# Optimization experiments

Measured on AMD Instinct MI355X. Metric: run time of the kernel, lower is better.

Reference implementation:

```python
import jax, jax.numpy as jnp
import numpy as np

WINDOW = (7, 7)
SHIFT = (3, 3)
NUM_HEADS = 4
DIM = 128


def _rel_pos_index():
    wh, ww = WINDOW
    coords = np.stack(np.meshgrid(np.arange(wh), np.arange(ww), indexing='ij'))  # [2,wh,ww]
    cf = coords.reshape(2, -1)                    # [2, N]
    rc = (cf[:, :, None] - cf[:, None, :]).transpose(1, 2, 0)  # [N,N,2]
    rc[:, :, 0] += wh - 1
    rc[:, :, 1] += ww - 1
    rc[:, :, 0] *= 2 * ww - 1
    return jnp.asarray(rc.sum(-1).reshape(-1))    # [N*N] int


def _attn_mask_np(pH, pW, sh):
    # Static-shape shift mask (host-side numpy; constant under jit).
    wh, ww = WINDOW
    m = np.zeros((pH, pW))
    h_slices = ((0, pH - wh), (pH - wh, pH - sh[0]), (pH - sh[0], pH))
    w_slices = ((0, pW - ww), (pW - ww, pW - sh[1]), (pW - sh[1], pW))
    cnt = 0
    for hs in h_slices:
        for ws in w_slices:
            m[hs[0]:hs[1], ws[0]:ws[1]] = cnt
            cnt += 1
    m = m.reshape(pH // wh, wh, pW // ww, ww).transpose(0, 2, 1, 3).reshape(-1, wh * ww)
    diff = m[:, None, :] - m[:, :, None]          # [num_windows, N, N]
    return jnp.asarray(np.where(diff != 0, -100.0, 0.0), dtype=np.float32)


def setup_inputs() -> dict:
    key = jax.random.key(0)
    ks = jax.random.split(key, 9)
    B, H, W, C = 32, 56, 56, DIM
    return {
        'input_q': jax.random.normal(ks[0], (B, H, W, C), jnp.float32),
        'input_k': jax.random.normal(ks[1], (B, H, W, C), jnp.float32),
        'input_v': jax.random.normal(ks[2], (B, H, W, C), jnp.float32),
        'q_weight': jax.random.normal(ks[3], (C, C), jnp.float32) * 0.05,
        'q_bias': jnp.zeros((C,), jnp.float32),
        'k_weight': jax.random.normal(ks[4], (C, C), jnp.float32) * 0.05,
        'k_bias': jnp.zeros((C,), jnp.float32),
        'v_weight': jax.random.normal(ks[5], (C, C), jnp.float32) * 0.05,
        'v_bias': jnp.zeros((C,), jnp.float32),
        'proj_weight': jax.random.normal(ks[6], (C, C), jnp.float32) * 0.05,
        'proj_bias': jnp.zeros((C,), jnp.float32),
        'rpb_table': jax.random.normal(ks[7], ((2 * WINDOW[0] - 1) * (2 * WINDOW[1] - 1), NUM_HEADS), jnp.float32) * 0.02,
    }


def reference(input_q, input_k, input_v, q_weight, q_bias, k_weight, k_bias,
              v_weight, v_bias, proj_weight, proj_bias, rpb_table):
    B, H, W, C = input_q.shape
    wh, ww = WINDOW
    pad_b = (wh - H % wh) % wh
    pad_r = (ww - W % ww) % ww
    pad = lambda t: jnp.pad(t, ((0, 0), (0, pad_b), (0, pad_r), (0, 0)))
    qx, kx, vx = pad(input_q), pad(input_k), pad(input_v)
    pad_H, pad_W = H + pad_b, W + pad_r
    sh = [0 if wh >= pad_H else SHIFT[0], 0 if ww >= pad_W else SHIFT[1]]
    if sum(sh) > 0:
        roll = lambda t: jnp.roll(t, (-sh[0], -sh[1]), axis=(1, 2))
        qx, kx, vx = roll(qx), roll(kx), roll(vx)
    nWh, nWw = pad_H // wh, pad_W // ww
    num_windows = nWh * nWw
    N = wh * ww

    def part(t):  # [B,pH,pW,C] -> [B*num_windows, N, C]
        t = t.reshape(B, nWh, wh, nWw, ww, C).transpose(0, 1, 3, 2, 4, 5)
        return t.reshape(B * num_windows, N, C)

    qx, kx, vx = part(qx), part(kx), part(vx)
    hd = C // NUM_HEADS

    def heads(x, w, b):  # linear + split heads -> [BW, nH, N, hd]
        return (x @ w.T + b).reshape(-1, N, NUM_HEADS, hd).transpose(0, 2, 1, 3)

    q = heads(qx, q_weight, q_bias) * (hd ** -0.5)
    k = heads(kx, k_weight, k_bias)
    v = heads(vx, v_weight, v_bias)

    attn = jnp.einsum('whqd,whkd->whqk', q, k)    # [BW, nH, N, N]
    rpb = rpb_table[_rel_pos_index()].reshape(N, N, NUM_HEADS).transpose(2, 0, 1)[None]
    attn = attn + rpb
    if sum(sh) > 0:
        mask = _attn_mask_np(pad_H, pad_W, sh)    # [num_windows, N, N]
        attn = attn.reshape(B, num_windows, NUM_HEADS, N, N) + mask[None, :, None]
        attn = attn.reshape(B * num_windows, NUM_HEADS, N, N)
    attn = jax.nn.softmax(attn, axis=-1)

    x = jnp.einsum('whqk,whkd->whqd', attn, v).transpose(0, 2, 1, 3).reshape(B * num_windows, N, C)
    x = x @ proj_weight.T + proj_bias
    x = x.reshape(B, nWh, nWw, wh, ww, C).transpose(0, 1, 3, 2, 4, 5).reshape(B, pad_H, pad_W, C)
    if sum(sh) > 0:
        x = jnp.roll(x, (sh[0], sh[1]), axis=(1, 2))
    return x[:, :H, :W, :]
```

## Files before the change

kernel.cpp:

```cpp
#include <hip/hip_runtime.h>

typedef __attribute__((ext_vector_type(8))) short s16x8;
typedef __attribute__((ext_vector_type(4))) float f32x4;
typedef __attribute__((ext_vector_type(4))) unsigned int u32x4;

#define MFMA16(a, b, c) __builtin_amdgcn_mfma_f32_16x16x32_bf16((a), (b), (c), 0, 0, 0)

static __device__ __forceinline__ unsigned short f2bf(float f) {
  unsigned int u = __float_as_uint(f);
  u += 0x7fffu + ((u >> 16) & 1u);
  return (unsigned short)(u >> 16);
}
static __device__ __forceinline__ int div7(int x) { return (x * 9363) >> 16; }
static __device__ __forceinline__ int swz256(int row, int byteoff) {
  return row * 256 + (byteoff ^ ((row & 7) << 4));
}
static __device__ __forceinline__ int swz128(int row, int byteoff) {
  return row * 128 + (byteoff ^ ((row & 7) << 4));
}

__global__ void swin_prep(const float* __restrict__ wq, const float* __restrict__ wk,
                          const float* __restrict__ wv, const float* __restrict__ wp,
                          const float* __restrict__ rpb_table,
                          unsigned short* __restrict__ wsW, float* __restrict__ rpbx) {
  int idx = blockIdx.x * 256 + threadIdx.x;
  if (idx < 65536) {
    int t = idx >> 14, loc = idx & 16383;
    const float* s = (t == 0) ? wq : (t == 1) ? wk : (t == 2) ? wv : wp;
    wsW[idx] = f2bf(s[loc]);
  } else {
    int k = idx - 65536;
    if (k < 4 * 49 * 49) {
      int h = k / 2401, rem = k - h * 2401;
      int i = rem / 49, j = rem - i * 49;
      int yi = i / 7, xi = i % 7, yj = j / 7, xj = j % 7;
      int ridx = (yi - yj + 6) * 13 + (xi - xj + 6);
      rpbx[k] = rpb_table[ridx * 4 + h];
    }
  }
}

__global__ __launch_bounds__(512, 4) void swin_main(
    const float* __restrict__ xq, const float* __restrict__ xk, const float* __restrict__ xv,
    const float* __restrict__ bq, const float* __restrict__ bk, const float* __restrict__ bv,
    const float* __restrict__ bp, const unsigned short* __restrict__ wsW,
    const float* __restrict__ rpbx, float* __restrict__ out) {
  __shared__ __align__(16) char sm[65536];

  const int tid = threadIdx.x;
  const int lane = tid & 63;
  const int wv_ = tid >> 6;
  const int l15 = lane & 15;
  const int lg = lane >> 4;
  const int kgrp = lg * 8;
  const int rsub = lg * 4;

  const int bid = blockIdx.x;
  const int b = bid >> 6;
  const int widx = bid & 63;
  const int wi = widx >> 3, wj = widx & 7;
  const long obase = (long)b * 56 * 56 * 128;

  const int xrow = tid >> 3;
  const int xk16 = (tid & 7) << 4;
  long xoff = -1;
  if (xrow < 49) {
    int ty = div7(xrow), tx = xrow - ty * 7;
    int ih = wi * 7 + ty + 3; if (ih >= 56) ih -= 56;
    int iw = wj * 7 + tx + 3; if (iw >= 56) iw -= 56;
    xoff = obase + (long)((ih * 56 + iw) * 128 + xk16);
  }
  float xr[16];
#pragma unroll
  for (int i = 0; i < 16; ++i) xr[i] = 0.f;

  auto issue_x = [&](const float* src) {
    if (xoff >= 0) {
      const float* p = src + xoff;
#pragma unroll
      for (int q = 0; q < 4; ++q) {
        f32x4 v = *(const f32x4*)(p + q * 4);
        xr[q * 4 + 0] = v[0]; xr[q * 4 + 1] = v[1];
        xr[q * 4 + 2] = v[2]; xr[q * 4 + 3] = v[3];
      }
    }
  };
  auto write_x = [&]() {
    unsigned int w[8];
#pragma unroll
    for (int i = 0; i < 8; ++i)
      w[i] = (unsigned int)f2bf(xr[2 * i]) | ((unsigned int)f2bf(xr[2 * i + 1]) << 16);
    u32x4 a = {w[0], w[1], w[2], w[3]};
    u32x4 bb = {w[4], w[5], w[6], w[7]};
    *(u32x4*)(sm + swz256(xrow, xk16 * 2)) = a;
    *(u32x4*)(sm + swz256(xrow, xk16 * 2 + 16)) = bb;
  };

  auto linear = [&](int woff, const float* bias, float scale, int mode, int dstbase) {
    const int n = wv_ * 16 + l15;
    s16x8 bfr[4];
#pragma unroll
    for (int kt = 0; kt < 4; ++kt)
      bfr[kt] = *(const s16x8*)(wsW + woff + n * 128 + kt * 32 + kgrp);
    float bval = bias[n] * scale;
#pragma unroll
    for (int mt = 0; mt < 4; ++mt) {
      f32x4 acc = {0.f, 0.f, 0.f, 0.f};
#pragma unroll
      for (int kt = 0; kt < 4; ++kt) {
        s16x8 afr = *(const s16x8*)(sm + swz256(mt * 16 + l15, (kt * 32 + kgrp) * 2));
        acc = MFMA16(afr, bfr[kt], acc);
      }
#pragma unroll
      for (int r = 0; r < 4; ++r) {
        float val = acc[r] * scale + bval;
        unsigned short h16 = f2bf(val);
        int row = mt * 16 + rsub + r;
        if (mode == 0)
          *(unsigned short*)(sm + dstbase + swz256(row, 2 * n)) = h16;
        else
          *(unsigned short*)(sm + 49152 + swz128(n, 2 * row)) = h16;
      }
    }
  };

  const float QSCALE = 0.17677669529663687f;

  issue_x(xq);
  write_x(); __syncthreads();
  issue_x(xk);
  linear(0, bq, QSCALE, 0, 16384); __syncthreads();
  write_x(); __syncthreads();
  issue_x(xv);
  linear(16384, bk, 1.f, 0, 32768); __syncthreads();
  write_x(); __syncthreads();
  linear(32768, bv, 1.f, 1, 0); __syncthreads();

  {
    const int h = wv_ & 3;
    const int half = wv_ >> 2;
    const int coff = h * 32;

    s16x8 kfr[4];
#pragma unroll
    for (int jt = 0; jt < 4; ++jt)
      kfr[jt] = *(const s16x8*)(sm + 32768 + swz256(jt * 16 + l15, (coff + kgrp) * 2));
    f32x4 S[2][4];
#pragma unroll
    for (int m2 = 0; m2 < 2; ++m2) {
      int mt = half * 2 + m2;
      s16x8 qfr = *(const s16x8*)(sm + 16384 + swz256(mt * 16 + l15, (coff + kgrp) * 2));
#pragma unroll
      for (int jt = 0; jt < 4; ++jt) {
        f32x4 z = {0.f, 0.f, 0.f, 0.f};
        S[m2][jt] = MFMA16(qfr, kfr[jt], z);
      }
    }

    const float* rpbh = rpbx + h * 2401;
    int jj[4], rgj[4]; bool jvld[4];
#pragma unroll
    for (int jt = 0; jt < 4; ++jt) {
      int j = jt * 16 + l15;
      jj[jt] = j; jvld[jt] = (j < 49);
      int jc = jvld[jt] ? j : 0;
      int yj = div7(jc), xj = jc - yj * 7;
      rgj[jt] = ((wi == 7) ? (yj < 4 ? 3 : 6) : 0) + ((wj == 7) ? (xj < 4 ? 1 : 2) : 0);
    }
#pragma unroll
    for (int m2 = 0; m2 < 2; ++m2) {
#pragma unroll
      for (int r = 0; r < 4; ++r) {
        int i = (half * 2 + m2) * 16 + rsub + r;
        if (i < 49) {
          int yi = div7(i), xi = i - yi * 7;
          int rgi = ((wi == 7) ? (yi < 4 ? 3 : 6) : 0) + ((wj == 7) ? (xi < 4 ? 1 : 2) : 0);
#pragma unroll
          for (int jt = 0; jt < 4; ++jt) {
            if (jvld[jt]) {
              float sv = S[m2][jt][r] + rpbh[i * 49 + jj[jt]];
              if (rgi != rgj[jt]) sv -= 100.f;
              S[m2][jt][r] = sv;
            } else {
              S[m2][jt][r] = -1e30f;
            }
          }
        } else {
#pragma unroll
          for (int jt = 0; jt < 4; ++jt)
            if (!jvld[jt]) S[m2][jt][r] = -1e30f;
        }
      }
    }

#pragma unroll
    for (int m2 = 0; m2 < 2; ++m2) {
#pragma unroll
      for (int r = 0; r < 4; ++r) {
        float m = fmaxf(fmaxf(S[m2][0][r], S[m2][1][r]), fmaxf(S[m2][2][r], S[m2][3][r]));
        for (int d = 1; d < 16; d <<= 1) m = fmaxf(m, __shfl_xor(m, d));
        float e0 = __expf(S[m2][0][r] - m);
        float e1 = __expf(S[m2][1][r] - m);
        float e2 = __expf(S[m2][2][r] - m);
        float e3 = __expf(S[m2][3][r] - m);
        float s = e0 + e1 + e2 + e3;
        for (int d = 1; d < 16; d <<= 1) s += __shfl_xor(s, d);
        float inv = 1.0f / s;
        S[m2][0][r] = e0 * inv; S[m2][1][r] = e1 * inv;
        S[m2][2][r] = e2 * inv; S[m2][3][r] = e3 * inv;
      }
    }
    __syncthreads();

    const int pbase = 16384 + h * 8192;
#pragma unroll
    for (int m2 = 0; m2 < 2; ++m2)
#pragma unroll
      for (int r = 0; r < 4; ++r) {
        int i = (half * 2 + m2) * 16 + rsub + r;
#pragma unroll
        for (int jt = 0; jt < 4; ++jt)
          *(unsigned short*)(sm + pbase + swz128(i, 2 * (jt * 16 + l15))) = f2bf(S[m2][jt][r]);
      }
    __syncthreads();

    s16x8 vfr[2][2];
#pragma unroll
    for (int ks = 0; ks < 2; ++ks)
#pragma unroll
      for (int nt = 0; nt < 2; ++nt) {
        int c = coff + nt * 16 + l15;
        vfr[ks][nt] = *(const s16x8*)(sm + 49152 + swz128(c, (ks * 32 + kgrp) * 2));
      }
    f32x4 Oacc[2][2];
#pragma unroll
    for (int m2 = 0; m2 < 2; ++m2)
#pragma unroll
      for (int nt = 0; nt < 2; ++nt) Oacc[m2][nt] = (f32x4){0.f, 0.f, 0.f, 0.f};
#pragma unroll
    for (int m2 = 0; m2 < 2; ++m2) {
#pragma unroll
      for (int ks = 0; ks < 2; ++ks) {
        s16x8 pfr = *(const s16x8*)(sm + pbase + swz128((half * 2 + m2) * 16 + l15, (ks * 32 + kgrp) * 2));
        Oacc[m2][0] = MFMA16(pfr, vfr[ks][0], Oacc[m2][0]);
        Oacc[m2][1] = MFMA16(pfr, vfr[ks][1], Oacc[m2][1]);
      }
    }
#pragma unroll
    for (int m2 = 0; m2 < 2; ++m2)
#pragma unroll
      for (int nt = 0; nt < 2; ++nt)
#pragma unroll
        for (int r = 0; r < 4; ++r) {
          int row = (half * 2 + m2) * 16 + rsub + r;
          int c = coff + nt * 16 + l15;
          *(unsigned short*)(sm + swz256(row, 2 * c)) = f2bf(Oacc[m2][nt][r]);
        }
    __syncthreads();
  }

  {
    const int woff = 49152;
    const int n = wv_ * 16 + l15;
    s16x8 bfr[4];
#pragma unroll
    for (int kt = 0; kt < 4; ++kt)
      bfr[kt] = *(const s16x8*)(wsW + woff + n * 128 + kt * 32 + kgrp);
    float bval = bp[n];
#pragma unroll
    for (int mt = 0; mt < 4; ++mt) {
      f32x4 acc = {0.f, 0.f, 0.f, 0.f};
#pragma unroll
      for (int kt = 0; kt < 4; ++kt) {
        s16x8 afr = *(const s16x8*)(sm + swz256(mt * 16 + l15, (kt * 32 + kgrp) * 2));
        acc = MFMA16(afr, bfr[kt], acc);
      }
#pragma unroll
      for (int r = 0; r < 4; ++r) {
        int tok = mt * 16 + rsub + r;
        if (tok < 49) {
          int ty = div7(tok), tx = tok - ty * 7;
          int oh = wi * 7 + ty + 3; if (oh >= 56) oh -= 56;
          int ow = wj * 7 + tx + 3; if (ow >= 56) ow -= 56;
          out[obase + (oh * 56 + ow) * 128 + n] = acc[r] + bval;
        }
      }
    }
  }
}

extern "C" void kernel_launch(void* const* d_in, const int* in_sizes, int n_in,
                              void* d_out, int out_size, void* d_ws, size_t ws_size,
                              hipStream_t stream) {
  const float* xq = (const float*)d_in[0];
  const float* xk = (const float*)d_in[1];
  const float* xv = (const float*)d_in[2];
  const float* wq = (const float*)d_in[3];
  const float* bq = (const float*)d_in[4];
  const float* wk = (const float*)d_in[5];
  const float* bk = (const float*)d_in[6];
  const float* wv = (const float*)d_in[7];
  const float* bv = (const float*)d_in[8];
  const float* wp = (const float*)d_in[9];
  const float* bp = (const float*)d_in[10];
  const float* rpb = (const float*)d_in[11];

  unsigned short* wsW = (unsigned short*)d_ws;
  float* rpbx = (float*)((char*)d_ws + 131072);

  swin_prep<<<294, 256, 0, stream>>>(wq, wk, wv, wp, rpb, wsW, rpbx);

  float* out = (float*)d_out;
  swin_main<<<2048, 512, 0, stream>>>(xq, xk, xv, bq, bk, bv, bp, wsW, rpbx, out);
}
```

Baseline: 90.65 us.

## Precompute padded bias+mask tables per window case and use exp2 softmax

The prep kernel now builds four padded 64x64 tables per head, one per shift-mask case. Each table folds together the relative position bias, the -100 shift mask, the padding sentinel and a log2(e) scale, so the main kernel only adds a preloaded value instead of computing region indices and branching. The Q scale also absorbs log2(e), so the softmax can use exp2f. The change also packs bf16 conversions in pairs with the hardware intrinsic, removes a barrier by moving the V projection into the attention scope, and hoists the bias loads ahead of the QK MFMAs. The trade-off is a larger bias table to read from global memory and more live registers for the preloaded values.

```diff
diff --git a/kernel.cpp b/kernel.cpp
--- a/kernel.cpp
+++ b/kernel.cpp
@@ -1,15 +1,18 @@
 #include <hip/hip_runtime.h>
+#include <hip/hip_bf16.h>
 
 typedef __attribute__((ext_vector_type(8))) short s16x8;
 typedef __attribute__((ext_vector_type(4))) float f32x4;
+typedef __attribute__((ext_vector_type(2))) unsigned int u32x2;
 typedef __attribute__((ext_vector_type(4))) unsigned int u32x4;
 
 #define MFMA16(a, b, c) __builtin_amdgcn_mfma_f32_16x16x32_bf16((a), (b), (c), 0, 0, 0)
-
-static __device__ __forceinline__ unsigned short f2bf(float f) {
-  unsigned int u = __float_as_uint(f);
-  u += 0x7fffu + ((u >> 16) & 1u);
-  return (unsigned short)(u >> 16);
+#define LOG2E 1.4426950408889634f
+
+static __device__ __forceinline__ unsigned int pk2(float a, float b) {
+  union { __hip_bfloat162 h2; unsigned int u; } cv;
+  cv.h2 = __float22bfloat162_rn(make_float2(a, b));
+  return cv.u;
 }
 static __device__ __forceinline__ int div7(int x) { return (x * 9363) >> 16; }
 static __device__ __forceinline__ int swz256(int row, int byteoff) {
@@ -22,21 +25,34 @@
 __global__ void swin_prep(const float* __restrict__ wq, const float* __restrict__ wk,
                           const float* __restrict__ wv, const float* __restrict__ wp,
                           const float* __restrict__ rpb_table,
-                          unsigned short* __restrict__ wsW, float* __restrict__ rpbx) {
+                          unsigned short* __restrict__ wsW, float* __restrict__ rpbm) {
   int idx = blockIdx.x * 256 + threadIdx.x;
   if (idx < 65536) {
     int t = idx >> 14, loc = idx & 16383;
     const float* s = (t == 0) ? wq : (t == 1) ? wk : (t == 2) ? wv : wp;
-    wsW[idx] = f2bf(s[loc]);
+    union { __hip_bfloat16 h; unsigned short u; } cv;
+    cv.h = __float2bfloat16(s[loc]);
+    wsW[idx] = cv.u;
   } else {
     int k = idx - 65536;
-    if (k < 4 * 49 * 49) {
-      int h = k / 2401, rem = k - h * 2401;
-      int i = rem / 49, j = rem - i * 49;
-      int yi = i / 7, xi = i % 7, yj = j / 7, xj = j % 7;
+    int c = k >> 14;
+    int h = (k >> 12) & 3;
+    int i = (k >> 6) & 63, j = k & 63;
+    float val;
+    if (j >= 49) val = -1e30f;
+    else if (i >= 49) val = 0.f;
+    else {
+      int yi = div7(i), xi = i - yi * 7;
+      int yj = div7(j), xj = j - yj * 7;
       int ridx = (yi - yj + 6) * 13 + (xi - xj + 6);
-      rpbx[k] = rpb_table[ridx * 4 + h];
-    }
+      val = rpb_table[ridx * 4 + h];
+      int cwi = c >> 1, cwj = c & 1;
+      int rgi = (cwi ? (yi < 4 ? 3 : 6) : 0) + (cwj ? (xi < 4 ? 1 : 2) : 0);
+      int rgj = (cwi ? (yj < 4 ? 3 : 6) : 0) + (cwj ? (xj < 4 ? 1 : 2) : 0);
+      if (rgi != rgj) val -= 100.f;
+      val *= LOG2E;
+    }
+    rpbm[k] = val;
   }
 }
 
@@ -44,7 +60,7 @@
     const float* __restrict__ xq, const float* __restrict__ xk, const float* __restrict__ xv,
     const float* __restrict__ bq, const float* __restrict__ bk, const float* __restrict__ bv,
     const float* __restrict__ bp, const unsigned short* __restrict__ wsW,
-    const float* __restrict__ rpbx, float* __restrict__ out) {
+    const float* __restrict__ rpbm, float* __restrict__ out) {
   __shared__ __align__(16) char sm[65536];
 
   const int tid = threadIdx.x;
@@ -60,6 +76,7 @@
   const int widx = bid & 63;
   const int wi = widx >> 3, wj = widx & 7;
   const long obase = (long)b * 56 * 56 * 128;
+  const int mcase = ((wi == 7) ? 2 : 0) + ((wj == 7) ? 1 : 0);
 
   const int xrow = tid >> 3;
   const int xk16 = (tid & 7) << 4;
@@ -88,13 +105,17 @@
   auto write_x = [&]() {
     unsigned int w[8];
 #pragma unroll
-    for (int i = 0; i < 8; ++i)
-      w[i] = (unsigned int)f2bf(xr[2 * i]) | ((unsigned int)f2bf(xr[2 * i + 1]) << 16);
+    for (int i = 0; i < 8; ++i) w[i] = pk2(xr[2 * i], xr[2 * i + 1]);
     u32x4 a = {w[0], w[1], w[2], w[3]};
     u32x4 bb = {w[4], w[5], w[6], w[7]};
     *(u32x4*)(sm + swz256(xrow, xk16 * 2)) = a;
     *(u32x4*)(sm + swz256(xrow, xk16 * 2 + 16)) = bb;
   };
+  auto st2 = [&](int a0, int a1, float v0, float v1) {
+    unsigned int u = pk2(v0, v1);
+    *(unsigned short*)(sm + a0) = (unsigned short)u;
+    *(unsigned short*)(sm + a1) = (unsigned short)(u >> 16);
+  };
 
   auto linear = [&](int woff, const float* bias, float scale, int mode, int dstbase) {
     const int n = wv_ * 16 + l15;
@@ -111,20 +132,20 @@
         s16x8 afr = *(const s16x8*)(sm + swz256(mt * 16 + l15, (kt * 32 + kgrp) * 2));
         acc = MFMA16(afr, bfr[kt], acc);
       }
-#pragma unroll
-      for (int r = 0; r < 4; ++r) {
-        float val = acc[r] * scale + bval;
-        unsigned short h16 = f2bf(val);
-        int row = mt * 16 + rsub + r;
-        if (mode == 0)
-          *(unsigned short*)(sm + dstbase + swz256(row, 2 * n)) = h16;
-        else
-          *(unsigned short*)(sm + 49152 + swz128(n, 2 * row)) = h16;
+      float v0 = acc[0] * scale + bval, v1 = acc[1] * scale + bval;
+      float v2 = acc[2] * scale + bval, v3 = acc[3] * scale + bval;
+      int row0 = mt * 16 + rsub;
+      if (mode == 0) {
+        st2(dstbase + swz256(row0, 2 * n), dstbase + swz256(row0 + 1, 2 * n), v0, v1);
+        st2(dstbase + swz256(row0 + 2, 2 * n), dstbase + swz256(row0 + 3, 2 * n), v2, v3);
+      } else {
+        u32x2 pkw = {pk2(v0, v1), pk2(v2, v3)};
+        *(u32x2*)(sm + 49152 + swz128(n, 2 * row0)) = pkw;
       }
     }
   };
 
-  const float QSCALE = 0.17677669529663687f;
+  const float QSCALE = 0.17677669529663687f * LOG2E;
 
   issue_x(xq);
   write_x(); __syncthreads();
@@ -134,18 +155,30 @@
   issue_x(xv);
   linear(16384, bk, 1.f, 0, 32768); __syncthreads();
   write_x(); __syncthreads();
-  linear(32768, bv, 1.f, 1, 0); __syncthreads();
-
+
+  const int h = wv_ & 3;
+  const int half = wv_ >> 2;
+  const int coff = h * 32;
+  f32x4 S[2][4];
   {
-    const int h = wv_ & 3;
-    const int half = wv_ >> 2;
-    const int coff = h * 32;
+    linear(32768, bv, 1.f, 1, 0);
+
+    const float* rpbm_h = rpbm + (((mcase << 2) + h) << 12);
+    float rv[2][4][4];
+#pragma unroll
+    for (int m2 = 0; m2 < 2; ++m2)
+#pragma unroll
+      for (int r = 0; r < 4; ++r) {
+        int i = (half * 2 + m2) * 16 + rsub + r;
+        const float* rp = rpbm_h + i * 64 + l15;
+#pragma unroll
+        for (int jt = 0; jt < 4; ++jt) rv[m2][jt][r] = rp[jt * 16];
+      }
 
     s16x8 kfr[4];
 #pragma unroll
     for (int jt = 0; jt < 4; ++jt)
       kfr[jt] = *(const s16x8*)(sm + 32768 + swz256(jt * 16 + l15, (coff + kgrp) * 2));
-    f32x4 S[2][4];
 #pragma unroll
     for (int m2 = 0; m2 < 2; ++m2) {
       int mt = half * 2 + m2;
@@ -157,41 +190,12 @@
       }
     }
 
-    const float* rpbh = rpbx + h * 2401;
-    int jj[4], rgj[4]; bool jvld[4];
-#pragma unroll
-    for (int jt = 0; jt < 4; ++jt) {
-      int j = jt * 16 + l15;
-      jj[jt] = j; jvld[jt] = (j < 49);
-      int jc = jvld[jt] ? j : 0;
-      int yj = div7(jc), xj = jc - yj * 7;
-      rgj[jt] = ((wi == 7) ? (yj < 4 ? 3 : 6) : 0) + ((wj == 7) ? (xj < 4 ? 1 : 2) : 0);
-    }
-#pragma unroll
-    for (int m2 = 0; m2 < 2; ++m2) {
-#pragma unroll
-      for (int r = 0; r < 4; ++r) {
-        int i = (half * 2 + m2) * 16 + rsub + r;
-        if (i < 49) {
-          int yi = div7(i), xi = i - yi * 7;
-          int rgi = ((wi == 7) ? (yi < 4 ? 3 : 6) : 0) + ((wj == 7) ? (xi < 4 ? 1 : 2) : 0);
-#pragma unroll
-          for (int jt = 0; jt < 4; ++jt) {
-            if (jvld[jt]) {
-              float sv = S[m2][jt][r] + rpbh[i * 49 + jj[jt]];
-              if (rgi != rgj[jt]) sv -= 100.f;
-              S[m2][jt][r] = sv;
-            } else {
-              S[m2][jt][r] = -1e30f;
-            }
-          }
-        } else {
-#pragma unroll
-          for (int jt = 0; jt < 4; ++jt)
-            if (!jvld[jt]) S[m2][jt][r] = -1e30f;
-        }
-      }
-    }
+#pragma unroll
+    for (int m2 = 0; m2 < 2; ++m2)
+#pragma unroll
+      for (int jt = 0; jt < 4; ++jt)
+#pragma unroll
+        for (int r = 0; r < 4; ++r) S[m2][jt][r] += rv[m2][jt][r];
 
 #pragma unroll
     for (int m2 = 0; m2 < 2; ++m2) {
@@ -199,10 +203,10 @@
       for (int r = 0; r < 4; ++r) {
         float m = fmaxf(fmaxf(S[m2][0][r], S[m2][1][r]), fmaxf(S[m2][2][r], S[m2][3][r]));
         for (int d = 1; d < 16; d <<= 1) m = fmaxf(m, __shfl_xor(m, d));
-        float e0 = __expf(S[m2][0][r] - m);
-        float e1 = __expf(S[m2][1][r] - m);
-        float e2 = __expf(S[m2][2][r] - m);
-        float e3 = __expf(S[m2][3][r] - m);
+        float e0 = exp2f(S[m2][0][r] - m);
+        float e1 = exp2f(S[m2][1][r] - m);
+        float e2 = exp2f(S[m2][2][r] - m);
+        float e3 = exp2f(S[m2][3][r] - m);
         float s = e0 + e1 + e2 + e3;
         for (int d = 1; d < 16; d <<= 1) s += __shfl_xor(s, d);
         float inv = 1.0f / s;
@@ -210,20 +214,23 @@
         S[m2][2][r] = e2 * inv; S[m2][3][r] = e3 * inv;
       }
     }
-    __syncthreads();
-
-    const int pbase = 16384 + h * 8192;
-#pragma unroll
-    for (int m2 = 0; m2 < 2; ++m2)
-#pragma unroll
-      for (int r = 0; r < 4; ++r) {
-        int i = (half * 2 + m2) * 16 + rsub + r;
-#pragma unroll
-        for (int jt = 0; jt < 4; ++jt)
-          *(unsigned short*)(sm + pbase + swz128(i, 2 * (jt * 16 + l15))) = f2bf(S[m2][jt][r]);
-      }
-    __syncthreads();
-
+  }
+  __syncthreads();
+
+  const int pbase = 16384 + h * 8192;
+#pragma unroll
+  for (int m2 = 0; m2 < 2; ++m2) {
+    int i0 = (half * 2 + m2) * 16 + rsub;
+#pragma unroll
+    for (int jt = 0; jt < 4; ++jt) {
+      int bo = 2 * (jt * 16 + l15);
+      st2(pbase + swz128(i0, bo), pbase + swz128(i0 + 1, bo), S[m2][jt][0], S[m2][jt][1]);
+      st2(pbase + swz128(i0 + 2, bo), pbase + swz128(i0 + 3, bo), S[m2][jt][2], S[m2][jt][3]);
+    }
+  }
+  __syncthreads();
+
+  {
     s16x8 vfr[2][2];
 #pragma unroll
     for (int ks = 0; ks < 2; ++ks)
@@ -247,25 +254,24 @@
       }
     }
 #pragma unroll
-    for (int m2 = 0; m2 < 2; ++m2)
-#pragma unroll
-      for (int nt = 0; nt < 2; ++nt)
-#pragma unroll
-        for (int r = 0; r < 4; ++r) {
-          int row = (half * 2 + m2) * 16 + rsub + r;
-          int c = coff + nt * 16 + l15;
-          *(unsigned short*)(sm + swz256(row, 2 * c)) = f2bf(Oacc[m2][nt][r]);
-        }
-    __syncthreads();
-  }
+    for (int m2 = 0; m2 < 2; ++m2) {
+      int row0 = (half * 2 + m2) * 16 + rsub;
+#pragma unroll
+      for (int nt = 0; nt < 2; ++nt) {
+        int c2 = 2 * (coff + nt * 16 + l15);
+        st2(swz256(row0, c2), swz256(row0 + 1, c2), Oacc[m2][nt][0], Oacc[m2][nt][1]);
+        st2(swz256(row0 + 2, c2), swz256(row0 + 3, c2), Oacc[m2][nt][2], Oacc[m2][nt][3]);
+      }
+    }
+  }
+  __syncthreads();
 
   {
-    const int woff = 49152;
     const int n = wv_ * 16 + l15;
     s16x8 bfr[4];
 #pragma unroll
     for (int kt = 0; kt < 4; ++kt)
-      bfr[kt] = *(const s16x8*)(wsW + woff + n * 128 + kt * 32 + kgrp);
+      bfr[kt] = *(const s16x8*)(wsW + 49152 + n * 128 + kt * 32 + kgrp);
     float bval = bp[n];
 #pragma unroll
     for (int mt = 0; mt < 4; ++mt) {
@@ -306,10 +312,10 @@
   const float* rpb = (const float*)d_in[11];
 
   unsigned short* wsW = (unsigned short*)d_ws;
-  float* rpbx = (float*)((char*)d_ws + 131072);
-
-  swin_prep<<<294, 256, 0, stream>>>(wq, wk, wv, wp, rpb, wsW, rpbx);
+  float* rpbm = (float*)((char*)d_ws + 131072);
+
+  swin_prep<<<512, 256, 0, stream>>>(wq, wk, wv, wp, rpb, wsW, rpbm);
 
   float* out = (float*)d_out;
-  swin_main<<<2048, 512, 0, stream>>>(xq, xk, xv, bq, bk, bv, bp, wsW, rpbx, out);
-}
+  swin_main<<<2048, 512, 0, stream>>>(xq, xk, xv, bq, bk, bv, bp, wsW, rpbm, out);
+}
```

New measurement: 81.22 us. 1.12x faster.
